# Kernel optimization log

Measured on AMD Instinct MI355X. Metric: run time of the kernel, lower is better.

Reference implementation:

```python
import jax, jax.numpy as jnp
import numpy as np

B, S, D = 2, 2048, 4096
H, KVH, HD = 32, 8, 128
ROPE_THETA = 10000.0

def setup_inputs() -> dict:
    key = jax.random.key(0)
    ks = jax.random.split(key, 5)
    x = jax.random.normal(ks[0], (B, S, D), jnp.float32)
    wq = jax.random.normal(ks[1], (D, H * HD), jnp.float32) * 0.02
    wk = jax.random.normal(ks[2], (D, KVH * HD), jnp.float32) * 0.02
    wv = jax.random.normal(ks[3], (D, KVH * HD), jnp.float32) * 0.02
    wo = jax.random.normal(ks[4], (H * HD, D), jnp.float32) * 0.02
    pos = jnp.arange(S, dtype=jnp.float32)
    inv_freq = 1.0 / (ROPE_THETA ** (jnp.arange(0, HD, 2, dtype=jnp.float32) / HD))
    freqs = pos[:, None] * inv_freq[None, :]  # [S, HD//2]
    return {"x": x, "cos": jnp.cos(freqs), "sin": jnp.sin(freqs),
            "wq": wq, "wk": wk, "wv": wv, "wo": wo, "start_pos": 0}

def _apply_rope(t, cos, sin):
    # t: [B, S, nh, HD]; rotate consecutive pairs (llama complex rotation)
    t = t.reshape(*t.shape[:-1], HD // 2, 2)
    t1, t2 = t[..., 0], t[..., 1]
    c = cos[None, :, None, :]
    s = sin[None, :, None, :]
    out = jnp.stack([t1 * c - t2 * s, t1 * s + t2 * c], axis=-1)
    return out.reshape(*out.shape[:-2], HD)

def reference(x, cos, sin, wq, wk, wv, wo, start_pos):
    b, s, _ = x.shape
    scale = 1.0 / np.sqrt(HD)
    xq = (x @ wq).reshape(b, s, H, HD)
    xk = (x @ wk).reshape(b, s, KVH, HD)
    xv = (x @ wv).reshape(b, s, KVH, HD)
    xq = _apply_rope(xq, cos, sin)
    xk = _apply_rope(xk, cos, sin)
    # start_pos == 0 prefill: cache write then read of [:s] is identity
    n_rep = H // KVH
    keys = jnp.repeat(xk, n_rep, axis=2)    # [b, s, H, HD]
    values = jnp.repeat(xv, n_rep, axis=2)
    q = xq.transpose(0, 2, 1, 3)            # [b, H, s, HD]
    k = keys.transpose(0, 2, 1, 3)
    v = values.transpose(0, 2, 1, 3)
    scores = jnp.einsum('bhqd,bhkd->bhqk', q, k) * scale
    mask = jnp.triu(jnp.full((s, s), -jnp.inf, dtype=scores.dtype), k=1)
    scores = scores + mask[None, None]
    attn = jax.nn.softmax(scores.astype(jnp.float32), axis=-1).astype(q.dtype)
    out = jnp.einsum('bhqk,bhkd->bhqd', attn, v)
    out = out.transpose(0, 2, 1, 3).reshape(b, s, H * HD)
    return out @ wo
```

## Files before the change

### kernel.cpp

```cpp
#include <hip/hip_runtime.h>

typedef __bf16 bf16_t;
typedef __bf16 bf16x8 __attribute__((ext_vector_type(8)));
typedef __bf16 bf16x4 __attribute__((ext_vector_type(4)));
typedef float  f32x4  __attribute__((ext_vector_type(4)));
typedef float  f32x16 __attribute__((ext_vector_type(16)));

#define NB   2
#define NS   2048
#define ND   4096
#define NH   32
#define NKVH 8
#define NHD  128

#define BAR()     asm volatile("s_barrier" ::: "memory")
#define LGKM0()   asm volatile("s_waitcnt lgkmcnt(0)" ::: "memory")
#define VMCNT10() asm volatile("s_waitcnt vmcnt(10)" ::: "memory")
#define VMCNT6()  asm volatile("s_waitcnt vmcnt(6)" ::: "memory")
#define VMCNT0()  asm volatile("s_waitcnt vmcnt(0)" ::: "memory")

__device__ __forceinline__ void gl_lds16(const bf16_t* g, bf16_t* l) {
  __builtin_amdgcn_global_load_lds(
      (const __attribute__((address_space(1))) void*)g,
      (__attribute__((address_space(3))) void*)l, 16, 0, 0);
}

__global__ void convert_f32_bf16(const float* __restrict__ in, bf16_t* __restrict__ out, int n4) {
  int i = blockIdx.x * 256 + threadIdx.x;
  if (i < n4) {
    f32x4 v = *(const f32x4*)&in[(size_t)i * 4];
    bf16x4 o;
    #pragma unroll
    for (int j = 0; j < 4; ++j) o[j] = (bf16_t)v[j];
    *(bf16x4*)&out[(size_t)i * 4] = o;
  }
}

__global__ void transpose_convert(const float* __restrict__ in, bf16_t* __restrict__ out, int Nin) {
  __shared__ float t[32][33];
  int tx = threadIdx.x & 31, ty = threadIdx.x >> 5;
  int n0 = blockIdx.x * 32, k0 = blockIdx.y * 32;
  #pragma unroll
  for (int i = 0; i < 4; ++i)
    t[ty + i * 8][tx] = in[(size_t)(k0 + ty + i * 8) * Nin + n0 + tx];
  __syncthreads();
  #pragma unroll
  for (int i = 0; i < 4; ++i)
    out[(size_t)(n0 + ty + i * 8) * 4096 + k0 + tx] = (bf16_t)t[tx][ty + i * 8];
}

__global__ __launch_bounds__(256, 2) void gemm192(const bf16_t* __restrict__ A,
                                                  const bf16_t* __restrict__ Bt,
                                                  bf16_t* __restrict__ C, int M, int N, int K) {
  __shared__ __align__(16) bf16_t As[2][128 * 64];
  __shared__ __align__(16) bf16_t Bs[2][192 * 64];
  const int tid = threadIdx.x, lane = tid & 63, wn = tid >> 6;
  const int l15 = lane & 15, l4 = lane >> 4;

  const int gx = gridDim.x;
  const int nwg = gx * gridDim.y;
  const int id = blockIdx.y * gx + blockIdx.x;
  const int wg = (id & 7) * (nwg >> 3) + (id >> 3);
  const int bx = wg % gx, by = wg / gx;
  const int row0 = bx * 128, col0 = by * 192;

  const bf16_t* Ab = A + (size_t)row0 * K;
  const bf16_t* Bb = Bt + (size_t)col0 * K;

  auto stA = [&](int t, int buf) {
    #pragma unroll
    for (int i = 0; i < 4; ++i) {
      int phys = i * 4096 + tid * 16;
      int logi = phys ^ (((phys >> 8) & 7) << 4);
      gl_lds16(Ab + (size_t)(logi >> 7) * K + t * 64 + ((logi & 127) >> 1),
               &As[buf][phys >> 1]);
    }
  };
  auto stB = [&](int t, int buf) {
    #pragma unroll
    for (int i = 0; i < 6; ++i) {
      int phys = i * 4096 + tid * 16;
      int logi = phys ^ (((phys >> 8) & 7) << 4);
      gl_lds16(Bb + (size_t)(logi >> 7) * K + t * 64 + ((logi & 127) >> 1),
               &Bs[buf][phys >> 1]);
    }
  };

  f32x4 acc[8][3];
  #pragma unroll
  for (int m = 0; m < 8; ++m)
    #pragma unroll
    for (int n = 0; n < 3; ++n)
      #pragma unroll
      for (int j = 0; j < 4; ++j) acc[m][n][j] = 0.f;

  const int nt = K >> 6;
  stA(0, 0); stB(0, 0);
  stA(1, 1); stB(1, 1);
  VMCNT10();
  BAR();

  auto ardA = [&](int buf, int mf, int kh) -> bf16x8 {
    int lb = (mf * 16 + l15) * 128 + kh * 64 + l4 * 16;
    return *(const bf16x8*)&As[buf][(lb ^ (((lb >> 8) & 7) << 4)) >> 1];
  };
  auto brdB = [&](int buf, int kh, int nf) -> bf16x8 {
    int lb = (wn * 48 + nf * 16 + l15) * 128 + kh * 64 + l4 * 16;
    return *(const bf16x8*)&Bs[buf][(lb ^ (((lb >> 8) & 7) << 4)) >> 1];
  };

  #pragma unroll 2
  for (int t = 0; t < nt; ++t) {
    const int cur = t & 1;
    bf16x8 a0[4][2], a1[4][2], b0[3], b1[3];

    #pragma unroll
    for (int mf = 0; mf < 4; ++mf)
      #pragma unroll
      for (int kh = 0; kh < 2; ++kh) a0[mf][kh] = ardA(cur, mf, kh);
    #pragma unroll
    for (int nf = 0; nf < 3; ++nf) b0[nf] = brdB(cur, 0, nf);
    #pragma unroll
    for (int nf = 0; nf < 3; ++nf) b1[nf] = brdB(cur, 1, nf);
    BAR();
    LGKM0();
    __builtin_amdgcn_s_setprio(1);
    #pragma unroll
    for (int mf = 0; mf < 4; ++mf)
      #pragma unroll
      for (int nf = 0; nf < 3; ++nf) {
        acc[mf][nf] = __builtin_amdgcn_mfma_f32_16x16x32_bf16(a0[mf][0], b0[nf], acc[mf][nf], 0, 0, 0);
        acc[mf][nf] = __builtin_amdgcn_mfma_f32_16x16x32_bf16(a0[mf][1], b1[nf], acc[mf][nf], 0, 0, 0);
      }
    __builtin_amdgcn_s_setprio(0);
    BAR();

    #pragma unroll
    for (int mf = 0; mf < 4; ++mf)
      #pragma unroll
      for (int kh = 0; kh < 2; ++kh) a1[mf][kh] = ardA(cur, 4 + mf, kh);
    if (t + 2 < nt) { stA(t + 2, cur); stB(t + 2, cur); }
    BAR();
    LGKM0();
    __builtin_amdgcn_s_setprio(1);
    #pragma unroll
    for (int mf = 0; mf < 4; ++mf)
      #pragma unroll
      for (int nf = 0; nf < 3; ++nf) {
        acc[4 + mf][nf] = __builtin_amdgcn_mfma_f32_16x16x32_bf16(a1[mf][0], b0[nf], acc[4 + mf][nf], 0, 0, 0);
        acc[4 + mf][nf] = __builtin_amdgcn_mfma_f32_16x16x32_bf16(a1[mf][1], b1[nf], acc[4 + mf][nf], 0, 0, 0);
      }
    __builtin_amdgcn_s_setprio(0);
    if (t + 2 < nt) { VMCNT10(); } else { VMCNT0(); }
    BAR();
  }

  #pragma unroll
  for (int mf = 0; mf < 8; ++mf)
    #pragma unroll
    for (int nf = 0; nf < 3; ++nf)
      #pragma unroll
      for (int r = 0; r < 4; ++r) {
        size_t row = (size_t)row0 + mf * 16 + l4 * 4 + r;
        size_t col = (size_t)col0 + wn * 48 + nf * 16 + l15;
        C[row * N + col] = (bf16_t)acc[mf][nf][r];
      }
}

__global__ __launch_bounds__(512, 2) void gemm256j(const bf16_t* __restrict__ A,
                                                   const bf16_t* __restrict__ Bt,
                                                   float* __restrict__ C, int M, int N, int K) {
  __shared__ __align__(16) bf16_t As[2][2][128 * 64];
  __shared__ __align__(16) bf16_t Bs[2][256 * 64];
  const int tid = threadIdx.x, lane = tid & 63, wid = tid >> 6;
  const int l15 = lane & 15, l4 = lane >> 4;
  const int wm = wid >> 2, wn = wid & 3;

  const int gx = gridDim.x;
  const int nwg = gx * gridDim.y;
  const int id = blockIdx.y * gx + blockIdx.x;
  const int wg = (id & 7) * (nwg >> 3) + (id >> 3);
  const int bx = wg % gx, by = wg / gx;
  const int row0 = bx * 256, col0 = by * 256;

  const bf16_t* Ab = A + (size_t)row0 * K;
  const bf16_t* Bb = Bt + (size_t)col0 * K;

  auto stA = [&](int t, int h, int buf) {
    #pragma unroll
    for (int i = 0; i < 2; ++i) {
      int phys = i * 8192 + tid * 16;
      int logi = phys ^ (((phys >> 8) & 7) << 4);
      gl_lds16(Ab + (size_t)(h * 128 + (logi >> 7)) * K + t * 64 + ((logi & 127) >> 1),
               &As[buf][h][phys >> 1]);
    }
  };
  auto stB = [&](int t, int buf) {
    #pragma unroll
    for (int i = 0; i < 4; ++i) {
      int phys = i * 8192 + tid * 16;
      int logi = phys ^ (((phys >> 8) & 7) << 4);
      gl_lds16(Bb + (size_t)(logi >> 7) * K + t * 64 + ((logi & 127) >> 1),
               &Bs[buf][phys >> 1]);
    }
  };

  f32x4 acc[8][4];
  #pragma unroll
  for (int m = 0; m < 8; ++m)
    #pragma unroll
    for (int n = 0; n < 4; ++n)
      #pragma unroll
      for (int j = 0; j < 4; ++j) acc[m][n][j] = 0.f;

  const int nt = K >> 6;
  stA(0, 0, 0); stA(0, 1, 0); stB(0, 0);
  stA(1, 0, 1); stB(1, 1);
  VMCNT6();
  BAR();

  auto ardA = [&](int buf, int mh, int kh, int mf) -> bf16x8 {
    int lb = (mh * 64 + mf * 16 + l15) * 128 + kh * 64 + l4 * 16;
    return *(const bf16x8*)&As[buf][wm][(lb ^ (((lb >> 8) & 7) << 4)) >> 1];
  };
  auto brdB = [&](int buf, int kh, int nf) -> bf16x8 {
    int lb = (wn * 64 + nf * 16 + l15) * 128 + kh * 64 + l4 * 16;
    return *(const bf16x8*)&Bs[buf][(lb ^ (((lb >> 8) & 7) << 4)) >> 1];
  };

  #pragma unroll 2
  for (int t = 0; t < nt; ++t) {
    const int cur = t & 1, nxt = cur ^ 1;
    bf16x8 a00[4], a01[4], a10[4], a11[4], b0[4], b1[4];

    #pragma unroll
    for (int mf = 0; mf < 4; ++mf) a00[mf] = ardA(cur, 0, 0, mf);
    #pragma unroll
    for (int nf = 0; nf < 4; ++nf) b0[nf] = brdB(cur, 0, nf);
    #pragma unroll
    for (int mf = 0; mf < 4; ++mf) a01[mf] = ardA(cur, 0, 1, mf);
    #pragma unroll
    for (int nf = 0; nf < 4; ++nf) b1[nf] = brdB(cur, 1, nf);
    if (t + 1 < nt) stA(t + 1, 1, nxt);
    BAR();
    LGKM0();
    __builtin_amdgcn_s_setprio(1);
    #pragma unroll
    for (int mf = 0; mf < 4; ++mf)
      #pragma unroll
      for (int nf = 0; nf < 4; ++nf)
        acc[mf][nf] = __builtin_amdgcn_mfma_f32_16x16x32_bf16(a00[mf], b0[nf], acc[mf][nf], 0, 0, 0);
    #pragma unroll
    for (int mf = 0; mf < 4; ++mf)
      #pragma unroll
      for (int nf = 0; nf < 4; ++nf)
        acc[mf][nf] = __builtin_amdgcn_mfma_f32_16x16x32_bf16(a01[mf], b1[nf], acc[mf][nf], 0, 0, 0);
    __builtin_amdgcn_s_setprio(0);
    BAR();

    #pragma unroll
    for (int mf = 0; mf < 4; ++mf) a10[mf] = ardA(cur, 1, 0, mf);
    #pragma unroll
    for (int mf = 0; mf < 4; ++mf) a11[mf] = ardA(cur, 1, 1, mf);
    if (t + 2 < nt) { stA(t + 2, 0, cur); stB(t + 2, cur); }
    BAR();
    LGKM0();
    __builtin_amdgcn_s_setprio(1);
    #pragma unroll
    for (int mf = 0; mf < 4; ++mf)
      #pragma unroll
      for (int nf = 0; nf < 4; ++nf)
        acc[4 + mf][nf] = __builtin_amdgcn_mfma_f32_16x16x32_bf16(a10[mf], b0[nf], acc[4 + mf][nf], 0, 0, 0);
    #pragma unroll
    for (int mf = 0; mf < 4; ++mf)
      #pragma unroll
      for (int nf = 0; nf < 4; ++nf)
        acc[4 + mf][nf] = __builtin_amdgcn_mfma_f32_16x16x32_bf16(a11[mf], b1[nf], acc[4 + mf][nf], 0, 0, 0);
    __builtin_amdgcn_s_setprio(0);
    if (t + 2 < nt) { VMCNT6(); } else { VMCNT0(); }
    BAR();
  }

  #pragma unroll
  for (int mh = 0; mh < 2; ++mh)
    #pragma unroll
    for (int mf = 0; mf < 4; ++mf)
      #pragma unroll
      for (int nf = 0; nf < 4; ++nf)
        #pragma unroll
        for (int r = 0; r < 4; ++r) {
          size_t row = (size_t)row0 + wm * 128 + mh * 64 + mf * 16 + l4 * 4 + r;
          size_t col = (size_t)col0 + wn * 64 + nf * 16 + l15;
          C[row * N + col] = acc[mh * 4 + mf][nf][r];
        }
}

__global__ void rope_qk(const bf16_t* __restrict__ qkv, const float* __restrict__ cosT,
                        const float* __restrict__ sinT, bf16_t* __restrict__ Q,
                        bf16_t* __restrict__ Kout) {
  int it = blockIdx.x * 256 + threadIdx.x;
  int chunk = it & 15;
  int hs = (it >> 4) % 40;
  int m = (it >> 4) / 40;
  int b = m >> 11, srow = m & 2047;

  bf16x8 v = *(const bf16x8*)&qkv[(size_t)m * 6144 + hs * 128 + chunk * 8];
  f32x4 c4 = *(const f32x4*)&cosT[(size_t)srow * 64 + chunk * 4];
  f32x4 s4 = *(const f32x4*)&sinT[(size_t)srow * 64 + chunk * 4];
  bf16x8 o;
  #pragma unroll
  for (int j = 0; j < 4; ++j) {
    float t1 = (float)v[2 * j], t2 = (float)v[2 * j + 1];
    o[2 * j]     = (bf16_t)(t1 * c4[j] - t2 * s4[j]);
    o[2 * j + 1] = (bf16_t)(t1 * s4[j] + t2 * c4[j]);
  }
  bf16_t* dst;
  if (hs < 32) dst = Q + (((size_t)(b * 32 + hs)) * 2048 + srow) * 128 + chunk * 8;
  else         dst = Kout + (((size_t)(b * 8 + (hs - 32))) * 2048 + srow) * 128 + chunk * 8;
  *(bf16x8*)dst = o;
}

__global__ void transpose_v(const bf16_t* __restrict__ qkv, bf16_t* __restrict__ Vt) {
  __shared__ bf16_t t[32][33];
  int tx = threadIdx.x & 31, ty = threadIdx.x >> 5;
  int s0 = blockIdx.x * 32, d0 = blockIdx.y * 32, g = blockIdx.z;
  int b = g >> 3, kv = g & 7;
  const bf16_t* src = qkv + (size_t)(b * 2048) * 6144 + 5120 + kv * 128;
  #pragma unroll
  for (int i = 0; i < 4; ++i)
    t[ty + i * 8][tx] = src[(size_t)(s0 + ty + i * 8) * 6144 + d0 + tx];
  __syncthreads();
  bf16_t* dst = Vt + (size_t)g * 128 * 2048;
  #pragma unroll
  for (int i = 0; i < 4; ++i)
    dst[(size_t)(d0 + ty + i * 8) * 2048 + s0 + tx] = t[tx][ty + i * 8];
}

__global__ __launch_bounds__(256, 2) void attn_kernel(const bf16_t* __restrict__ Q,
                                                      const bf16_t* __restrict__ Kc,
                                                      const bf16_t* __restrict__ Vt,
                                                      bf16_t* __restrict__ Oout) {
  __shared__ __align__(16) bf16_t Ks[2][64 * 128];
  __shared__ __align__(16) bf16_t Vs[2][128 * 64];

  const int tid = threadIdx.x, wid = tid >> 6, lane = tid & 63;
  const int l31 = lane & 31, hi = lane >> 5;
  const int bh = blockIdx.y;
  const int b = bh >> 5, h = bh & 31, kv = h >> 2;
  const int pr = blockIdx.x;

  const bf16_t* Qp = Q + ((size_t)bh * 2048) * 128;
  const bf16_t* Kp = Kc + ((size_t)(b * 8 + kv) * 2048) * 128;
  const bf16_t* Vp = Vt + ((size_t)(b * 8 + kv) * 128) * 2048;

  const float kscale = 0.08838834764831845f * 1.44269504088896f;

  auto stage = [&](int kt, int buf) {
    const int k0 = kt * 64;
    #pragma unroll
    for (int i = 0; i < 4; ++i) {
      int phys = i * 4096 + tid * 16;
      int logi = phys ^ (((phys >> 8) & 15) << 4);
      gl_lds16(Kp + (size_t)(k0 + (phys >> 8)) * 128 + ((logi & 255) >> 1), &Ks[buf][phys >> 1]);
    }
    #pragma unroll
    for (int i = 0; i < 4; ++i) {
      int phys = i * 4096 + tid * 16;
      int logi = phys ^ (((phys >> 7) & 7) << 4);
      gl_lds16(Vp + (size_t)(phys >> 7) * 2048 + k0 + ((logi & 127) >> 1), &Vs[buf][phys >> 1]);
    }
  };

  for (int half = 0; half < 2; ++half) {
    const int qt = half ? pr : 15 - pr;
    const int q0b = qt * 128;
    const int q0w = q0b + wid * 32;
    const int qg = q0w + l31;
    const int nkt = (qt + 1) * 2;

    bf16x8 qf[8];
    #pragma unroll
    for (int c = 0; c < 8; ++c) {
      bf16x8 t = *(const bf16x8*)&Qp[(size_t)qg * 128 + c * 16 + hi * 8];
      #pragma unroll
      for (int j = 0; j < 8; ++j) t[j] = (bf16_t)((float)t[j] * kscale);
      qf[c] = t;
    }

    f32x16 oa[4];
    #pragma unroll
    for (int nc = 0; nc < 4; ++nc)
      #pragma unroll
      for (int r = 0; r < 16; ++r) oa[nc][r] = 0.f;
    float m_old = -1e30f, lrow = 0.f;

    stage(0, 0);
    __syncthreads();

    for (int kt = 0; kt < nkt; ++kt) {
      const int k0 = kt * 64, cur = kt & 1;
      if (kt + 1 < nkt) stage(kt + 1, cur ^ 1);

      if (k0 <= q0w + 31) {
        f32x16 s0, s1;
        #pragma unroll
        for (int r = 0; r < 16; ++r) { s0[r] = 0.f; s1[r] = 0.f; }
        __builtin_amdgcn_s_setprio(1);
        #pragma unroll
        for (int c = 0; c < 8; ++c) {
          int lb0 = l31 * 256 + c * 32 + hi * 16;
          int pb0 = lb0 ^ (((lb0 >> 8) & 15) << 4);
          bf16x8 kf0 = *(const bf16x8*)&Ks[cur][pb0 >> 1];
          s0 = __builtin_amdgcn_mfma_f32_32x32x16_bf16(kf0, qf[c], s0, 0, 0, 0);
          int lb1 = (32 + l31) * 256 + c * 32 + hi * 16;
          int pb1 = lb1 ^ (((lb1 >> 8) & 15) << 4);
          bf16x8 kf1 = *(const bf16x8*)&Ks[cur][pb1 >> 1];
          s1 = __builtin_amdgcn_mfma_f32_32x32x16_bf16(kf1, qf[c], s1, 0, 0, 0);
        }
        __builtin_amdgcn_s_setprio(0);

        if (k0 + 63 > q0w) {
          #pragma unroll
          for (int r = 0; r < 16; ++r) {
            int key0 = k0 + ((r & 3) + 8 * (r >> 2)) + 4 * hi;
            if (key0 > qg) s0[r] = -1e30f;
            if (key0 + 32 > qg) s1[r] = -1e30f;
          }
        }

        float m8[8];
        #pragma unroll
        for (int j = 0; j < 8; ++j)
          m8[j] = fmaxf(fmaxf(s0[j], s0[j + 8]), fmaxf(s1[j], s1[j + 8]));
        float ma = fmaxf(fmaxf(m8[0], m8[4]), fmaxf(m8[1], m8[5]));
        float mb = fmaxf(fmaxf(m8[2], m8[6]), fmaxf(m8[3], m8[7]));
        float mh = fmaxf(ma, mb);
        float mfull = fmaxf(mh, __shfl_xor(mh, 32));
        float mn = fmaxf(m_old, mfull);
        bool nores = (mfull <= m_old);
        float sc = exp2f(m_old - mn);
        m_old = mn;

        if (!__all((int)nores)) {
          #pragma unroll
          for (int r = 0; r < 16; ++r) {
            int qi = (r & 3) + 8 * (r >> 2) + 4 * hi;
            float scv = __int_as_float(__builtin_amdgcn_ds_bpermute(qi << 2, __float_as_int(sc)));
            oa[0][r] *= scv; oa[1][r] *= scv; oa[2][r] *= scv; oa[3][r] *= scv;
          }
        }

        #pragma unroll
        for (int r = 0; r < 16; ++r) {
          s0[r] = exp2f(s0[r] - mn);
          s1[r] = exp2f(s1[r] - mn);
        }
        float rsA = 0.f, rsB = 0.f, rsC = 0.f, rsD = 0.f;
        #pragma unroll
        for (int r = 0; r < 16; r += 4) {
          rsA += s0[r];     rsB += s0[r + 1]; rsC += s0[r + 2]; rsD += s0[r + 3];
          rsA += s1[r];     rsB += s1[r + 1]; rsC += s1[r + 2]; rsD += s1[r + 3];
        }
        float rs = (rsA + rsB) + (rsC + rsD);
        rs += __shfl_xor(rs, 32);
        lrow = lrow * sc + rs;

        #pragma unroll
        for (int ks = 0; ks < 4; ++ks) {
          const int qi0 = (ks & 1) * 8;
          union { bf16_t hh[4]; int ii[2]; } ku, su;
          #pragma unroll
          for (int j = 0; j < 4; ++j) {
            float lo, hv;
            if (ks >> 1) { lo = s1[qi0 + j]; hv = s1[qi0 + 4 + j]; }
            else         { lo = s0[qi0 + j]; hv = s0[qi0 + 4 + j]; }
            ku.hh[j] = (bf16_t)(hi ? hv : lo);
            su.hh[j] = (bf16_t)(hi ? lo : hv);
          }
          int r0 = __shfl_xor(su.ii[0], 32), r1 = __shfl_xor(su.ii[1], 32);
          union { int ii[4]; bf16x8 v; } fa;
          fa.ii[0] = hi ? r0 : ku.ii[0];
          fa.ii[1] = hi ? r1 : ku.ii[1];
          fa.ii[2] = hi ? ku.ii[0] : r0;
          fa.ii[3] = hi ? ku.ii[1] : r1;
          __builtin_amdgcn_s_setprio(1);
          #pragma unroll
          for (int nc = 0; nc < 4; ++nc) {
            int lb = (nc * 32 + l31) * 128 + ks * 32 + hi * 16;
            int pb = lb ^ (((lb >> 7) & 7) << 4);
            bf16x8 vf = *(const bf16x8*)&Vs[cur][pb >> 1];
            oa[nc] = __builtin_amdgcn_mfma_f32_32x32x16_bf16(fa.v, vf, oa[nc], 0, 0, 0);
          }
          __builtin_amdgcn_s_setprio(0);
        }
      }
      __syncthreads();
    }

    float inv = 1.0f / lrow;
    bf16_t* Op = Oout + ((size_t)(b * 2048 + q0w)) * 4096 + (size_t)h * 128;
    #pragma unroll
    for (int r = 0; r < 16; ++r) {
      int qi = (r & 3) + 8 * (r >> 2) + 4 * hi;
      float iv = __int_as_float(__builtin_amdgcn_ds_bpermute(qi << 2, __float_as_int(inv)));
      #pragma unroll
      for (int nc = 0; nc < 4; ++nc)
        Op[(size_t)qi * 4096 + nc * 32 + l31] = (bf16_t)(oa[nc][r] * iv);
    }
  }
}

extern "C" void kernel_launch(void* const* d_in, const int* in_sizes, int n_in,
                              void* d_out, int out_size, void* d_ws, size_t ws_size,
                              hipStream_t stream) {
  const float* x    = (const float*)d_in[0];
  const float* cosT = (const float*)d_in[1];
  const float* sinT = (const float*)d_in[2];
  const float* wq   = (const float*)d_in[3];
  const float* wk   = (const float*)d_in[4];
  const float* wv   = (const float*)d_in[5];
  const float* wo   = (const float*)d_in[6];
  float* out = (float*)d_out;
  char* ws = (char*)d_ws;

  bf16_t* wqkvT = (bf16_t*)(ws + 0);
  bf16_t* woT   = wqkvT;
  bf16_t* xb    = (bf16_t*)(ws + 50331648);
  bf16_t* Qb    = xb;
  bf16_t* qkv   = (bf16_t*)(ws + 83886080);
  bf16_t* attn_out = qkv;
  bf16_t* Kb    = (bf16_t*)(ws + 134217728);
  bf16_t* Vt    = (bf16_t*)(ws + 142606336);

  convert_f32_bf16<<<16384, 256, 0, stream>>>(x, xb, 4194304);
  transpose_convert<<<dim3(128, 128), 256, 0, stream>>>(wq, wqkvT, 4096);
  transpose_convert<<<dim3(32, 128), 256, 0, stream>>>(wk, wqkvT + (size_t)4096 * 4096, 1024);
  transpose_convert<<<dim3(32, 128), 256, 0, stream>>>(wv, wqkvT + (size_t)5120 * 4096, 1024);

  gemm192<<<dim3(32, 32), 256, 0, stream>>>(xb, wqkvT, qkv, 4096, 6144, 4096);

  transpose_convert<<<dim3(128, 128), 256, 0, stream>>>(wo, woT, 4096);
  rope_qk<<<10240, 256, 0, stream>>>(qkv, cosT, sinT, Qb, Kb);
  transpose_v<<<dim3(64, 4, 16), 256, 0, stream>>>(qkv, Vt);

  attn_kernel<<<dim3(8, 64), 256, 0, stream>>>(Qb, Kb, Vt, attn_out);

  gemm256j<<<dim3(16, 16), 512, 0, stream>>>(attn_out, woT, out, 4096, 4096, 4096);
}
```

Before: 526.8 us.

## Use 2x2 wave tiling in QKV GEMM and lazy softmax rescaling in attention

The bf16 GEMM changes each wave's tile from a full 128x48 strip to a 64x96 block on a 2x2 wave grid. This cuts LDS reads per MFMA because A fragments are shared across six N fragments. The loop now loads only one k-half of B per phase instead of a second set of A fragments. The flash attention loop also skips rescaling the output accumulator and the running sum unless the new max exceeds the old one by more than 8 in log2 units. This removes most bpermute/multiply rescale passes, at the cost of exp2 values up to 2^8 that bf16/fp32 should tolerate.

```diff
diff --git a/kernel.cpp b/kernel.cpp
--- a/kernel.cpp
+++ b/kernel.cpp
@@ -54,8 +54,9 @@
                                                   bf16_t* __restrict__ C, int M, int N, int K) {
   __shared__ __align__(16) bf16_t As[2][128 * 64];
   __shared__ __align__(16) bf16_t Bs[2][192 * 64];
-  const int tid = threadIdx.x, lane = tid & 63, wn = tid >> 6;
+  const int tid = threadIdx.x, lane = tid & 63, wid = tid >> 6;
   const int l15 = lane & 15, l4 = lane >> 4;
+  const int wm = wid >> 1, wn = wid & 1;
 
   const int gx = gridDim.x;
   const int nwg = gx * gridDim.y;
@@ -86,11 +87,11 @@
     }
   };
 
-  f32x4 acc[8][3];
-  #pragma unroll
-  for (int m = 0; m < 8; ++m)
-    #pragma unroll
-    for (int n = 0; n < 3; ++n)
+  f32x4 acc[4][6];
+  #pragma unroll
+  for (int m = 0; m < 4; ++m)
+    #pragma unroll
+    for (int n = 0; n < 6; ++n)
       #pragma unroll
       for (int j = 0; j < 4; ++j) acc[m][n][j] = 0.f;
 
@@ -101,44 +102,38 @@
   BAR();
 
   auto ardA = [&](int buf, int mf, int kh) -> bf16x8 {
-    int lb = (mf * 16 + l15) * 128 + kh * 64 + l4 * 16;
+    int lb = (wm * 64 + mf * 16 + l15) * 128 + kh * 64 + l4 * 16;
     return *(const bf16x8*)&As[buf][(lb ^ (((lb >> 8) & 7) << 4)) >> 1];
   };
   auto brdB = [&](int buf, int kh, int nf) -> bf16x8 {
-    int lb = (wn * 48 + nf * 16 + l15) * 128 + kh * 64 + l4 * 16;
+    int lb = (wn * 96 + nf * 16 + l15) * 128 + kh * 64 + l4 * 16;
     return *(const bf16x8*)&Bs[buf][(lb ^ (((lb >> 8) & 7) << 4)) >> 1];
   };
 
   #pragma unroll 2
   for (int t = 0; t < nt; ++t) {
     const int cur = t & 1;
-    bf16x8 a0[4][2], a1[4][2], b0[3], b1[3];
-
-    #pragma unroll
-    for (int mf = 0; mf < 4; ++mf)
-      #pragma unroll
-      for (int kh = 0; kh < 2; ++kh) a0[mf][kh] = ardA(cur, mf, kh);
-    #pragma unroll
-    for (int nf = 0; nf < 3; ++nf) b0[nf] = brdB(cur, 0, nf);
-    #pragma unroll
-    for (int nf = 0; nf < 3; ++nf) b1[nf] = brdB(cur, 1, nf);
+    bf16x8 a[4][2], b0[6], b1[6];
+
+    #pragma unroll
+    for (int mf = 0; mf < 4; ++mf)
+      #pragma unroll
+      for (int kh = 0; kh < 2; ++kh) a[mf][kh] = ardA(cur, mf, kh);
+    #pragma unroll
+    for (int nf = 0; nf < 6; ++nf) b0[nf] = brdB(cur, 0, nf);
     BAR();
     LGKM0();
     __builtin_amdgcn_s_setprio(1);
     #pragma unroll
     for (int mf = 0; mf < 4; ++mf)
       #pragma unroll
-      for (int nf = 0; nf < 3; ++nf) {
-        acc[mf][nf] = __builtin_amdgcn_mfma_f32_16x16x32_bf16(a0[mf][0], b0[nf], acc[mf][nf], 0, 0, 0);
-        acc[mf][nf] = __builtin_amdgcn_mfma_f32_16x16x32_bf16(a0[mf][1], b1[nf], acc[mf][nf], 0, 0, 0);
-      }
+      for (int nf = 0; nf < 6; ++nf)
+        acc[mf][nf] = __builtin_amdgcn_mfma_f32_16x16x32_bf16(a[mf][0], b0[nf], acc[mf][nf], 0, 0, 0);
     __builtin_amdgcn_s_setprio(0);
     BAR();
 
     #pragma unroll
-    for (int mf = 0; mf < 4; ++mf)
-      #pragma unroll
-      for (int kh = 0; kh < 2; ++kh) a1[mf][kh] = ardA(cur, 4 + mf, kh);
+    for (int nf = 0; nf < 6; ++nf) b1[nf] = brdB(cur, 1, nf);
     if (t + 2 < nt) { stA(t + 2, cur); stB(t + 2, cur); }
     BAR();
     LGKM0();
@@ -146,23 +141,21 @@
     #pragma unroll
     for (int mf = 0; mf < 4; ++mf)
       #pragma unroll
-      for (int nf = 0; nf < 3; ++nf) {
-        acc[4 + mf][nf] = __builtin_amdgcn_mfma_f32_16x16x32_bf16(a1[mf][0], b0[nf], acc[4 + mf][nf], 0, 0, 0);
-        acc[4 + mf][nf] = __builtin_amdgcn_mfma_f32_16x16x32_bf16(a1[mf][1], b1[nf], acc[4 + mf][nf], 0, 0, 0);
-      }
+      for (int nf = 0; nf < 6; ++nf)
+        acc[mf][nf] = __builtin_amdgcn_mfma_f32_16x16x32_bf16(a[mf][1], b1[nf], acc[mf][nf], 0, 0, 0);
     __builtin_amdgcn_s_setprio(0);
     if (t + 2 < nt) { VMCNT10(); } else { VMCNT0(); }
     BAR();
   }
 
   #pragma unroll
-  for (int mf = 0; mf < 8; ++mf)
-    #pragma unroll
-    for (int nf = 0; nf < 3; ++nf)
+  for (int mf = 0; mf < 4; ++mf)
+    #pragma unroll
+    for (int nf = 0; nf < 6; ++nf)
       #pragma unroll
       for (int r = 0; r < 4; ++r) {
-        size_t row = (size_t)row0 + mf * 16 + l4 * 4 + r;
-        size_t col = (size_t)col0 + wn * 48 + nf * 16 + l15;
+        size_t row = (size_t)row0 + wm * 64 + mf * 16 + l4 * 4 + r;
+        size_t col = (size_t)col0 + wn * 96 + nf * 16 + l15;
         C[row * N + col] = (bf16_t)acc[mf][nf][r];
       }
 }
@@ -436,18 +429,22 @@
         float mb = fmaxf(fmaxf(m8[2], m8[6]), fmaxf(m8[3], m8[7]));
         float mh = fmaxf(ma, mb);
         float mfull = fmaxf(mh, __shfl_xor(mh, 32));
-        float mn = fmaxf(m_old, mfull);
-        bool nores = (mfull <= m_old);
-        float sc = exp2f(m_old - mn);
-        m_old = mn;
-
-        if (!__all((int)nores)) {
+
+        float mn;
+        bool defer = (mfull - m_old <= 8.0f);
+        if (__all((int)defer)) {
+          mn = m_old;
+        } else {
+          mn = fmaxf(m_old, mfull);
+          float sc = exp2f(m_old - mn);
           #pragma unroll
           for (int r = 0; r < 16; ++r) {
             int qi = (r & 3) + 8 * (r >> 2) + 4 * hi;
             float scv = __int_as_float(__builtin_amdgcn_ds_bpermute(qi << 2, __float_as_int(sc)));
             oa[0][r] *= scv; oa[1][r] *= scv; oa[2][r] *= scv; oa[3][r] *= scv;
           }
+          lrow *= sc;
+          m_old = mn;
         }
 
         #pragma unroll
@@ -463,7 +460,7 @@
         }
         float rs = (rsA + rsB) + (rsC + rsD);
         rs += __shfl_xor(rs, 32);
-        lrow = lrow * sc + rs;
+        lrow = lrow + rs;
 
         #pragma unroll
         for (int ks = 0; ks < 4; ++ks) {
```

Result: faster. 513.2 us (-2.6%).
